# Optimization experiments

Measured on AMD Instinct MI355X. Metric: run time of the kernel, lower is better.

## Reference

```python
import jax, jax.numpy as jnp
import numpy as np

LEAK = 0.2
NUM_GRAPHS = 64


def _gat(h_in, src, dst, eh, W, att_src, att_dst, att_edge, lin_edge_W, bias, N):
    # PyG GATConv with edge_dim, concat=False (mean over heads)
    H, C = att_src.shape
    h = (h_in @ W).reshape(N, H, C)                      # [N,H,C]
    e = (eh @ lin_edge_W).reshape(-1, H, C)              # [Eaug,H,C]
    a_s = jnp.einsum('nhc,hc->nh', h, att_src)           # [N,H]
    a_d = jnp.einsum('nhc,hc->nh', h, att_dst)
    a_e = jnp.einsum('ehc,hc->eh', e, att_edge)          # [Eaug,H]
    score = jax.nn.leaky_relu(a_s[src] + a_d[dst] + a_e, LEAK)
    # scatter-softmax over incoming edges of each destination node
    m = jax.ops.segment_max(score, dst, num_segments=N)
    ex = jnp.exp(score - m[dst])
    den = jax.ops.segment_sum(ex, dst, num_segments=N)
    alpha = ex / den[dst]                                # [Eaug,H]
    out = jax.ops.segment_sum(alpha[:, :, None] * h[src], dst, num_segments=N)
    return out.mean(axis=1) + bias                       # concat=False -> head mean


def setup_inputs() -> dict:
    key = jax.random.key(0)
    ks = jax.random.split(key, 32)
    N, E, F, FE, HID, H, NT = 30000, 480000, 64, 16, 64, 4, 16
    Cin1 = F + HID
    s = 0.05
    d = {
        'x': jax.random.normal(ks[0], (N, F), jnp.float32),
        'edge_attr': jax.random.normal(ks[1], (E, FE), jnp.float32),
        'node_emb': jax.random.normal(ks[2], (NT, HID), jnp.float32) * s,
        'edge_W': jax.random.normal(ks[3], (FE, HID), jnp.float32) * s,
        'edge_b': jnp.zeros((HID,), jnp.float32),
        'W1': jax.random.normal(ks[4], (Cin1, H * HID), jnp.float32) * s,
        'as1': jax.random.normal(ks[5], (H, HID), jnp.float32) * s,
        'ad1': jax.random.normal(ks[6], (H, HID), jnp.float32) * s,
        'ae1': jax.random.normal(ks[7], (H, HID), jnp.float32) * s,
        'leW1': jax.random.normal(ks[8], (HID, H * HID), jnp.float32) * s,
        'b1': jnp.zeros((HID,), jnp.float32),
        'W2': jax.random.normal(ks[9], (HID, H * HID), jnp.float32) * s,
        'as2': jax.random.normal(ks[10], (H, HID), jnp.float32) * s,
        'ad2': jax.random.normal(ks[11], (H, HID), jnp.float32) * s,
        'ae2': jax.random.normal(ks[12], (H, HID), jnp.float32) * s,
        'leW2': jax.random.normal(ks[13], (HID, H * HID), jnp.float32) * s,
        'b2': jnp.zeros((HID,), jnp.float32),
        'sage_Wl': jax.random.normal(ks[14], (HID, HID), jnp.float32) * s,
        'sage_bl': jnp.zeros((HID,), jnp.float32),
        'sage_Wr': jax.random.normal(ks[15], (HID, HID), jnp.float32) * s,
        'lin1_W': jax.random.normal(ks[16], (HID, HID), jnp.float32) * s,
        'lin1_b': jnp.zeros((HID,), jnp.float32),
        'lin2_W': jax.random.normal(ks[17], (HID, HID), jnp.float32) * s,
        'lin2_b': jnp.zeros((HID,), jnp.float32),
        'tel_W': jax.random.normal(ks[18], (HID, 1), jnp.float32) * s,
        'tel_b': jnp.zeros((1,), jnp.float32),
        'comp_W': jax.random.normal(ks[19], (HID, 1), jnp.float32) * s,
        'comp_b': jnp.zeros((1,), jnp.float32),
        'pch_W': jax.random.normal(ks[20], (HID, 1), jnp.float32) * s,
        'pch_b': jnp.zeros((1,), jnp.float32),
        'edge_index': jax.random.randint(ks[21], (2, E), 0, N, jnp.int32),
        'batch': jnp.sort(jax.random.randint(ks[22], (N,), 0, NUM_GRAPHS, jnp.int32)),
        'node_type': jax.random.randint(ks[23], (N,), 0, NT, jnp.int32),
    }
    return d


def reference(x, edge_attr, node_emb, edge_W, edge_b,
              W1, as1, ad1, ae1, leW1, b1,
              W2, as2, ad2, ae2, leW2, b2,
              sage_Wl, sage_bl, sage_Wr,
              lin1_W, lin1_b, lin2_W, lin2_b,
              tel_W, tel_b, comp_W, comp_b, pch_W, pch_b,
              edge_index, batch, node_type):
    N = x.shape[0]
    src0, dst0 = edge_index[0], edge_index[1]

    h0 = jnp.concatenate([x, node_emb[node_type]], axis=-1)   # [N, F+HID]
    eh = edge_attr @ edge_W + edge_b                          # [E, HID]

    # GATConv default add_self_loops=True, fill_value='mean' on edge_attr
    loop = jnp.arange(N, dtype=src0.dtype)
    src = jnp.concatenate([src0, loop])
    dst = jnp.concatenate([dst0, loop])
    eh_aug = jnp.concatenate([eh, jnp.broadcast_to(eh.mean(axis=0), (N, eh.shape[1]))], axis=0)

    h1 = jax.nn.elu(_gat(h0, src, dst, eh_aug, W1, as1, ad1, ae1, leW1, b1, N))
    h2 = jax.nn.elu(_gat(h1, src, dst, eh_aug, W2, as2, ad2, ae2, leW2, b2, N))

    # SAGEConv: mean neighbor aggregation (src->dst) + root transform
    deg = jax.ops.segment_sum(jnp.ones_like(dst0, dtype=h2.dtype), dst0, num_segments=N)
    agg = jax.ops.segment_sum(h2[src0], dst0, num_segments=N) / jnp.clip(deg, 1.0)[:, None]
    h3 = jax.nn.elu(agg @ sage_Wl + sage_bl + h2 @ sage_Wr)

    # global mean pool per graph
    cnt = jax.ops.segment_sum(jnp.ones((N,), h3.dtype), batch, num_segments=NUM_GRAPHS)
    g = jax.ops.segment_sum(h3, batch, num_segments=NUM_GRAPHS) / jnp.clip(cnt, 1.0)[:, None]

    g = jax.nn.elu(g @ lin1_W + lin1_b)                       # dropout inactive (eval)
    g = g @ lin2_W + lin2_b
    return (g @ tel_W + tel_b, g @ comp_W + comp_b, g @ pch_W + pch_b)
```

## Files before the change

### kernel.cpp

```cpp
#include <hip/hip_runtime.h>
#include <math.h>

#define NN 30000
#define NE 480000
#define FEA 16
#define HID 64
#define NG 64
#define LEAKK 0.2f

#define S_MEANEA 0
#define S_KF1    16
#define S_C1     80
#define S_AEL1   84
#define S_KF2    88
#define S_C2     152
#define S_AEL2   156
#define S_MS1    160
#define S_MD1    672
#define S_MS2    1184
#define S_MD2    1440

__device__ __forceinline__ float eluf(float v) { return v > 0.f ? v : expm1f(v); }
__device__ __forceinline__ float leakyf(float v) { return v >= 0.f ? v : LEAKK * v; }
__device__ __forceinline__ void fma4(float4& a, float w, const float4& x) {
    a.x += w * x.x; a.y += w * x.y; a.z += w * x.z; a.w += w * x.w;
}

__global__ __launch_bounds__(256) void count_mean_kernel(
    const int* __restrict__ dst, const float* __restrict__ EA,
    int* __restrict__ cnt, float* __restrict__ S) {
    __shared__ float red[1024];
    int t = threadIdx.x;
    int base = blockIdx.x * 512;
#pragma unroll
    for (int i = 0; i < 2; i++) {
        int e = base + i * 256 + t;
        if (e < NE) atomicAdd(&cnt[dst[e]], 1);
    }
    int c4 = t & 3;
    int rbase = base + (t >> 2);
    float4 acc = {0, 0, 0, 0};
#pragma unroll
    for (int i = 0; i < 8; i++) {
        int r = rbase + i * 64;
        if (r < NE) {
            float4 v = *(const float4*)(EA + (size_t)r * FEA + c4 * 4);
            acc.x += v.x; acc.y += v.y; acc.z += v.z; acc.w += v.w;
        }
    }
    *(float4*)&red[t * 4] = acc;
    __syncthreads();
    if (t < 16) {
        int grp = t >> 2;
        int comp = t & 3;
        float sum = 0.f;
        for (int j = 0; j < 64; j++) sum += red[(grp + 4 * j) * 4 + comp];
        atomicAdd(&S[S_MEANEA + grp * 4 + comp], sum);
    }
}

__global__ void prep_weights_kernel(const float* __restrict__ W1, const float* __restrict__ W2,
                                    const float* __restrict__ Wl, const float* __restrict__ Wr,
                                    const float* __restrict__ emb,
                                    float* __restrict__ WC1, float* __restrict__ WC2,
                                    float* __restrict__ B128) {
    int i = blockIdx.x * 256 + threadIdx.x;
    if (i < 16384) {
        int hk = i >> 6, c = i & 63;
        int h = hk >> 6, k = hk & 63;
        WC1[i] = 0.25f * W1[k * 256 + h * 64 + c];
    } else if (i < 20480) {
        int j2 = i - 16384;
        int r2 = j2 >> 6, c = j2 & 63;
        int h = r2 >> 4, tau = r2 & 15;
        float v = 0.f;
        for (int j = 0; j < 64; j++)
            v += emb[tau * 64 + j] * W1[(64 + j) * 256 + h * 64 + c];
        WC1[i] = 0.25f * v;
    } else if (i < 36864) {
        int j = i - 20480;
        int hk = j >> 6, c = j & 63;
        int h = hk >> 6, k = hk & 63;
        WC2[j] = 0.25f * W2[k * 256 + h * 64 + c];
    } else if (i < 45056) {
        int j = i - 36864;
        int k = j >> 6, c = j & 63;
        B128[j] = (k < 64) ? Wl[k * 64 + c] : Wr[(k - 64) * 64 + c];
    }
}

__global__ void prep_small_kernel(
    const float* __restrict__ W1, const float* __restrict__ as1, const float* __restrict__ ad1,
    const float* __restrict__ ae1, const float* __restrict__ leW1,
    const float* __restrict__ W2, const float* __restrict__ as2, const float* __restrict__ ad2,
    const float* __restrict__ ae2, const float* __restrict__ leW2,
    const float* __restrict__ edge_W, const float* __restrict__ edge_b,
    float* __restrict__ S) {
    __shared__ float M1[256], M2[256], meh[64];
    int t = threadIdx.x;
    if (t < 16) S[S_MEANEA + t] *= (1.0f / (float)NE);
    __syncthreads();
    {
        int k = t >> 2, h = t & 3;
        float m1 = 0.f, m2 = 0.f;
        for (int c = 0; c < 64; c++) {
            m1 += leW1[k * 256 + h * 64 + c] * ae1[h * 64 + c];
            m2 += leW2[k * 256 + h * 64 + c] * ae2[h * 64 + c];
        }
        M1[t] = m1; M2[t] = m2;
    }
    if (t < 64) {
        float v = edge_b[t];
        for (int f = 0; f < FEA; f++) v += S[S_MEANEA + f] * edge_W[f * 64 + t];
        meh[t] = v;
    }
    __syncthreads();
    if (t < 64) {
        int f = t >> 2, h = t & 3;
        float k1 = 0.f, k2 = 0.f;
        for (int k = 0; k < 64; k++) {
            k1 += edge_W[f * 64 + k] * M1[k * 4 + h];
            k2 += edge_W[f * 64 + k] * M2[k * 4 + h];
        }
        S[S_KF1 + t] = k1; S[S_KF2 + t] = k2;
    } else if (t < 68) {
        int h = t - 64;
        float c1 = 0.f, c2 = 0.f, a1 = 0.f, a2 = 0.f;
        for (int k = 0; k < 64; k++) {
            c1 += edge_b[k] * M1[k * 4 + h];
            c2 += edge_b[k] * M2[k * 4 + h];
            a1 += meh[k] * M1[k * 4 + h];
            a2 += meh[k] * M2[k * 4 + h];
        }
        S[S_C1 + h] = c1; S[S_C2 + h] = c2;
        S[S_AEL1 + h] = a1; S[S_AEL2 + h] = a2;
    }
    for (int i = t; i < 512; i += 256) {
        int k = i >> 2, h = i & 3;
        float s = 0.f, d = 0.f;
        for (int c = 0; c < 64; c++) {
            float w = W1[k * 256 + h * 64 + c];
            s += w * as1[h * 64 + c];
            d += w * ad1[h * 64 + c];
        }
        S[S_MS1 + i] = s; S[S_MD1 + i] = d;
    }
    for (int i = t; i < 256; i += 256) {
        int k = i >> 2, h = i & 3;
        float s = 0.f, d = 0.f;
        for (int c = 0; c < 64; c++) {
            float w = W2[k * 256 + h * 64 + c];
            s += w * as2[h * 64 + c];
            d += w * ad2[h * 64 + c];
        }
        S[S_MS2 + i] = s; S[S_MD2 + i] = d;
    }
}

__global__ __launch_bounds__(256) void attn_h0_kernel(
    const float* __restrict__ x, const float* __restrict__ node_emb,
    const int* __restrict__ node_type, const float* __restrict__ S,
    float* __restrict__ as_, float* __restrict__ ad_) {
    __shared__ float xt[64 * 132];
    __shared__ float ms[512], md[512];
    __shared__ int ntS[64];
    int t = threadIdx.x;
    int n0 = blockIdx.x * 64;
    if (t < 64) {
        int n = n0 + t;
        ntS[t] = (n < NN) ? node_type[n] : 0;
    }
    for (int i = t; i < 512; i += 256) { ms[i] = S[S_MS1 + i]; md[i] = S[S_MD1 + i]; }
    __syncthreads();
    for (int i = t; i < 1024; i += 256) {
        int r = i >> 4, c4 = (i & 15) * 4;
        int n = n0 + r;
        float4 f = {0, 0, 0, 0};
        if (n < NN) f = *(const float4*)(x + (size_t)n * 64 + c4);
        *(float4*)&xt[r * 132 + c4] = f;
    }
    for (int i = t; i < 1024; i += 256) {
        int r = i >> 4, c4 = (i & 15) * 4;
        int n = n0 + r;
        float4 f = {0, 0, 0, 0};
        if (n < NN) f = *(const float4*)(node_emb + (size_t)ntS[r] * 64 + c4);
        *(float4*)&xt[r * 132 + 64 + c4] = f;
    }
    __syncthreads();
    int r = t >> 2, h = t & 3;
    float s = 0.f, d = 0.f;
#pragma unroll 8
    for (int k = 0; k < 128; k++) {
        float xv = xt[r * 132 + k];
        s += xv * ms[k * 4 + h];
        d += xv * md[k * 4 + h];
    }
    int n = n0 + r;
    if (n < NN) { as_[n * 4 + h] = s; ad_[n * 4 + h] = d; }
}

__global__ void scan_blocks_kernel(const int* __restrict__ cnt, int* __restrict__ eoff,
                                   int* __restrict__ bsum) {
    __shared__ int wsum[16];
    int t = threadIdx.x;
    int i = blockIdx.x * 1024 + t;
    int v = (i < NN) ? cnt[i] : 0;
    int lane = t & 63;
    int incl = v;
#pragma unroll
    for (int ofs = 1; ofs < 64; ofs <<= 1) {
        int u = __shfl_up(incl, ofs, 64);
        if (lane >= ofs) incl += u;
    }
    int wid = t >> 6;
    if (lane == 63) wsum[wid] = incl;
    __syncthreads();
    if (t < 16) {
        int s = wsum[t];
#pragma unroll
        for (int ofs = 1; ofs < 16; ofs <<= 1) {
            int u = __shfl_up(s, ofs, 64);
            if (t >= ofs) s += u;
        }
        wsum[t] = s;
    }
    __syncthreads();
    int excl = incl - v + (wid > 0 ? wsum[wid - 1] : 0);
    if (i < NN) eoff[i] = excl;
    if (t == 1023) bsum[blockIdx.x] = excl + v;
}

__global__ void scan_tops_kernel(const int* __restrict__ bsum, int* __restrict__ boff, int nb) {
    int t = threadIdx.x;
    int v = (t < nb) ? bsum[t] : 0;
    int incl = v;
#pragma unroll
    for (int ofs = 1; ofs < 64; ofs <<= 1) {
        int u = __shfl_up(incl, ofs, 64);
        if (t >= ofs) incl += u;
    }
    boff[t] = incl - v;
}

__global__ void scan_add_kernel(const int* __restrict__ boff, int* __restrict__ eoff) {
    int i = blockIdx.x * 256 + threadIdx.x;
    if (i < NN) eoff[i] += boff[i >> 10];
    if (i == 0) eoff[NN] = NE;
}

__global__ void scatter_score_kernel(const int* __restrict__ src, const int* __restrict__ dst,
                                     const float* __restrict__ EA, const float* __restrict__ S,
                                     const float* __restrict__ as_, const float* __restrict__ ad_,
                                     const int* __restrict__ node_type,
                                     const int* __restrict__ eoff, int* __restrict__ pos,
                                     int2* __restrict__ se_sorted,
                                     float* __restrict__ sc1, float* __restrict__ ae2s) {
    int e = blockIdx.x * 256 + threadIdx.x;
    if (e >= NE) return;
    int s = src[e], d = dst[e];
    float a1[4], a2[4];
#pragma unroll
    for (int h = 0; h < 4; h++) { a1[h] = S[S_C1 + h]; a2[h] = S[S_C2 + h]; }
    const float4* EA4 = (const float4*)(EA + (size_t)e * FEA);
#pragma unroll
    for (int q = 0; q < 4; q++) {
        float4 v = EA4[q];
        float vv[4] = {v.x, v.y, v.z, v.w};
#pragma unroll
        for (int j = 0; j < 4; j++) {
            int f = q * 4 + j;
#pragma unroll
            for (int h = 0; h < 4; h++) {
                a1[h] += vv[j] * S[S_KF1 + f * 4 + h];
                a2[h] += vv[j] * S[S_KF2 + f * 4 + h];
            }
        }
    }
    ((float4*)ae2s)[e] = make_float4(a2[0], a2[1], a2[2], a2[3]);
    float4 asv = ((const float4*)as_)[s];
    float4 adv = ((const float4*)ad_)[d];
    float4 r;
    r.x = expf(leakyf(asv.x + adv.x + a1[0]));
    r.y = expf(leakyf(asv.y + adv.y + a1[1]));
    r.z = expf(leakyf(asv.z + adv.z + a1[2]));
    r.w = expf(leakyf(asv.w + adv.w + a1[3]));
    ((float4*)sc1)[e] = r;
    int ty = node_type[s];
    int p = atomicAdd(&pos[d], 1);
    se_sorted[eoff[d] + p] = make_int2(s, e | (ty << 24));
}

__global__ void goff_bs_kernel(const int* __restrict__ batch, int* __restrict__ goff) {
    int g = threadIdx.x;
    if (g > NG) return;
    int lo = 0, hi = NN;
    while (lo < hi) {
        int mid = (lo + hi) >> 1;
        if (batch[mid] < g) lo = mid + 1; else hi = mid;
    }
    goff[g] = lo;
}

__global__ __launch_bounds__(256) void agg_gat1_kernel(
    const int* __restrict__ eoff, const int2* __restrict__ se_sorted,
    const float* __restrict__ sc1, const float* __restrict__ x,
    const int* __restrict__ node_type,
    const float* __restrict__ as_, const float* __restrict__ ad_,
    const float* __restrict__ Sael, float* __restrict__ agg) {
    int n = blockIdx.x * 4 + (threadIdx.x >> 6);
    if (n >= NN) return;
    int lane = threadIdx.x & 63;
    int sub = lane >> 4, ch = lane & 15;
    const float4* X4 = (const float4*)x;
    const float4* W4 = (const float4*)sc1;
    float4 asn = ((const float4*)as_)[n];
    float4 adn = ((const float4*)ad_)[n];
    float4 a0 = {0, 0, 0, 0}, a1 = a0, a2 = a0, a3 = a0, dn = a0, tw = a0;
    int b = eoff[n], e_end = eoff[n + 1];
    int nE = e_end - b;
    int i = sub;
    for (; i + 4 < nE; i += 8) {
        int2 se0 = se_sorted[b + i], se1 = se_sorted[b + i + 4];
        int e0 = se0.y & 0xFFFFFF, t0 = se0.y >> 24;
        int e1 = se1.y & 0xFFFFFF, t1 = se1.y >> 24;
        float4 w0 = W4[e0], w1 = W4[e1];
        float4 x0 = X4[(size_t)se0.x * 16 + ch];
        float4 x1 = X4[(size_t)se1.x * 16 + ch];
        fma4(a0, w0.x, x0); fma4(a1, w0.y, x0); fma4(a2, w0.z, x0); fma4(a3, w0.w, x0);
        fma4(a0, w1.x, x1); fma4(a1, w1.y, x1); fma4(a2, w1.z, x1); fma4(a3, w1.w, x1);
        dn.x += w0.x + w1.x; dn.y += w0.y + w1.y;
        dn.z += w0.z + w1.z; dn.w += w0.w + w1.w;
        if (ch == t0) { tw.x += w0.x; tw.y += w0.y; tw.z += w0.z; tw.w += w0.w; }
        if (ch == t1) { tw.x += w1.x; tw.y += w1.y; tw.z += w1.z; tw.w += w1.w; }
    }
    for (; i < nE; i += 4) {
        int2 se0 = se_sorted[b + i];
        int e0 = se0.y & 0xFFFFFF, t0 = se0.y >> 24;
        float4 w0 = W4[e0];
        float4 x0 = X4[(size_t)se0.x * 16 + ch];
        fma4(a0, w0.x, x0); fma4(a1, w0.y, x0); fma4(a2, w0.z, x0); fma4(a3, w0.w, x0);
        dn.x += w0.x; dn.y += w0.y; dn.z += w0.z; dn.w += w0.w;
        if (ch == t0) { tw.x += w0.x; tw.y += w0.y; tw.z += w0.z; tw.w += w0.w; }
    }
    if (sub == 0) {
        float e0 = expf(leakyf(asn.x + adn.x + Sael[0]));
        float e1 = expf(leakyf(asn.y + adn.y + Sael[1]));
        float e2 = expf(leakyf(asn.z + adn.z + Sael[2]));
        float e3 = expf(leakyf(asn.w + adn.w + Sael[3]));
        float4 xs = X4[(size_t)n * 16 + ch];
        fma4(a0, e0, xs); fma4(a1, e1, xs); fma4(a2, e2, xs); fma4(a3, e3, xs);
        dn.x += e0; dn.y += e1; dn.z += e2; dn.w += e3;
        int tn = node_type[n];
        if (ch == tn) { tw.x += e0; tw.y += e1; tw.z += e2; tw.w += e3; }
    }
#pragma unroll
    for (int mask = 16; mask < 64; mask <<= 1) {
        a0.x += __shfl_xor(a0.x, mask, 64); a0.y += __shfl_xor(a0.y, mask, 64);
        a0.z += __shfl_xor(a0.z, mask, 64); a0.w += __shfl_xor(a0.w, mask, 64);
        a1.x += __shfl_xor(a1.x, mask, 64); a1.y += __shfl_xor(a1.y, mask, 64);
        a1.z += __shfl_xor(a1.z, mask, 64); a1.w += __shfl_xor(a1.w, mask, 64);
        a2.x += __shfl_xor(a2.x, mask, 64); a2.y += __shfl_xor(a2.y, mask, 64);
        a2.z += __shfl_xor(a2.z, mask, 64); a2.w += __shfl_xor(a2.w, mask, 64);
        a3.x += __shfl_xor(a3.x, mask, 64); a3.y += __shfl_xor(a3.y, mask, 64);
        a3.z += __shfl_xor(a3.z, mask, 64); a3.w += __shfl_xor(a3.w, mask, 64);
        dn.x += __shfl_xor(dn.x, mask, 64); dn.y += __shfl_xor(dn.y, mask, 64);
        dn.z += __shfl_xor(dn.z, mask, 64); dn.w += __shfl_xor(dn.w, mask, 64);
        tw.x += __shfl_xor(tw.x, mask, 64); tw.y += __shfl_xor(tw.y, mask, 64);
        tw.z += __shfl_xor(tw.z, mask, 64); tw.w += __shfl_xor(tw.w, mask, 64);
    }
    if (sub == 0) {
        float i0 = 1.f / dn.x, i1 = 1.f / dn.y, i2 = 1.f / dn.z, i3 = 1.f / dn.w;
        float* A = agg + (size_t)n * 320;
        float4* A4 = (float4*)A;
        A4[ch]      = make_float4(a0.x * i0, a0.y * i0, a0.z * i0, a0.w * i0);
        A4[16 + ch] = make_float4(a1.x * i1, a1.y * i1, a1.z * i1, a1.w * i1);
        A4[32 + ch] = make_float4(a2.x * i2, a2.y * i2, a2.z * i2, a2.w * i2);
        A4[48 + ch] = make_float4(a3.x * i3, a3.y * i3, a3.z * i3, a3.w * i3);
        A[256 + ch]      = tw.x * i0;
        A[256 + 16 + ch] = tw.y * i1;
        A[256 + 32 + ch] = tw.z * i2;
        A[256 + 48 + ch] = tw.w * i3;
    }
}

__global__ __launch_bounds__(256) void agg_gat2_kernel(
    const int* __restrict__ eoff, const int2* __restrict__ se_sorted,
    const float* __restrict__ ae2s, const float* __restrict__ X,
    const float* __restrict__ as_, const float* __restrict__ ad_,
    const float* __restrict__ Sael, float* __restrict__ agg) {
    int n = blockIdx.x * 4 + (threadIdx.x >> 6);
    if (n >= NN) return;
    int lane = threadIdx.x & 63;
    int sub = lane >> 4, ch = lane & 15;
    const float4* X4 = (const float4*)X;
    const float4* W4 = (const float4*)ae2s;
    const float4* AS4 = (const float4*)as_;
    float4 asn = AS4[n];
    float4 adn = ((const float4*)ad_)[n];
    float4 a0 = {0, 0, 0, 0}, a1 = a0, a2 = a0, a3 = a0, dn = a0;
    int b = eoff[n], e = eoff[n + 1];
    int nE = e - b;
    int i = sub;
    for (; i + 4 < nE; i += 8) {
        int2 se0 = se_sorted[b + i], se1 = se_sorted[b + i + 4];
        float4 w0 = W4[se0.y & 0xFFFFFF], w1 = W4[se1.y & 0xFFFFFF];
        float4 q0 = AS4[se0.x], q1 = AS4[se1.x];
        w0.x = expf(leakyf(q0.x + adn.x + w0.x));
        w0.y = expf(leakyf(q0.y + adn.y + w0.y));
        w0.z = expf(leakyf(q0.z + adn.z + w0.z));
        w0.w = expf(leakyf(q0.w + adn.w + w0.w));
        w1.x = expf(leakyf(q1.x + adn.x + w1.x));
        w1.y = expf(leakyf(q1.y + adn.y + w1.y));
        w1.z = expf(leakyf(q1.z + adn.z + w1.z));
        w1.w = expf(leakyf(q1.w + adn.w + w1.w));
        float4 x0 = X4[(size_t)se0.x * 16 + ch];
        float4 x1 = X4[(size_t)se1.x * 16 + ch];
        fma4(a0, w0.x, x0); fma4(a1, w0.y, x0); fma4(a2, w0.z, x0); fma4(a3, w0.w, x0);
        fma4(a0, w1.x, x1); fma4(a1, w1.y, x1); fma4(a2, w1.z, x1); fma4(a3, w1.w, x1);
        dn.x += w0.x + w1.x; dn.y += w0.y + w1.y;
        dn.z += w0.z + w1.z; dn.w += w0.w + w1.w;
    }
    for (; i < nE; i += 4) {
        int2 se0 = se_sorted[b + i];
        float4 w0 = W4[se0.y & 0xFFFFFF];
        float4 q0 = AS4[se0.x];
        w0.x = expf(leakyf(q0.x + adn.x + w0.x));
        w0.y = expf(leakyf(q0.y + adn.y + w0.y));
        w0.z = expf(leakyf(q0.z + adn.z + w0.z));
        w0.w = expf(leakyf(q0.w + adn.w + w0.w));
        float4 x0 = X4[(size_t)se0.x * 16 + ch];
        fma4(a0, w0.x, x0); fma4(a1, w0.y, x0); fma4(a2, w0.z, x0); fma4(a3, w0.w, x0);
        dn.x += w0.x; dn.y += w0.y; dn.z += w0.z; dn.w += w0.w;
    }
    if (sub == 0) {
        float e0 = expf(leakyf(asn.x + adn.x + Sael[0]));
        float e1 = expf(leakyf(asn.y + adn.y + Sael[1]));
        float e2 = expf(leakyf(asn.z + adn.z + Sael[2]));
        float e3 = expf(leakyf(asn.w + adn.w + Sael[3]));
        float4 xs = X4[(size_t)n * 16 + ch];
        fma4(a0, e0, xs); fma4(a1, e1, xs); fma4(a2, e2, xs); fma4(a3, e3, xs);
        dn.x += e0; dn.y += e1; dn.z += e2; dn.w += e3;
    }
#pragma unroll
    for (int mask = 16; mask < 64; mask <<= 1) {
        a0.x += __shfl_xor(a0.x, mask, 64); a0.y += __shfl_xor(a0.y, mask, 64);
        a0.z += __shfl_xor(a0.z, mask, 64); a0.w += __shfl_xor(a0.w, mask, 64);
        a1.x += __shfl_xor(a1.x, mask, 64); a1.y += __shfl_xor(a1.y, mask, 64);
        a1.z += __shfl_xor(a1.z, mask, 64); a1.w += __shfl_xor(a1.w, mask, 64);
        a2.x += __shfl_xor(a2.x, mask, 64); a2.y += __shfl_xor(a2.y, mask, 64);
        a2.z += __shfl_xor(a2.z, mask, 64); a2.w += __shfl_xor(a2.w, mask, 64);
        a3.x += __shfl_xor(a3.x, mask, 64); a3.y += __shfl_xor(a3.y, mask, 64);
        a3.z += __shfl_xor(a3.z, mask, 64); a3.w += __shfl_xor(a3.w, mask, 64);
        dn.x += __shfl_xor(dn.x, mask, 64); dn.y += __shfl_xor(dn.y, mask, 64);
        dn.z += __shfl_xor(dn.z, mask, 64); dn.w += __shfl_xor(dn.w, mask, 64);
    }
    if (sub == 0) {
        float i0 = 1.f / dn.x, i1 = 1.f / dn.y, i2 = 1.f / dn.z, i3 = 1.f / dn.w;
        float4* agg4 = (float4*)(agg + (size_t)n * 256);
        agg4[ch]      = make_float4(a0.x * i0, a0.y * i0, a0.z * i0, a0.w * i0);
        agg4[16 + ch] = make_float4(a1.x * i1, a1.y * i1, a1.z * i1, a1.w * i1);
        agg4[32 + ch] = make_float4(a2.x * i2, a2.y * i2, a2.z * i2, a2.w * i2);
        agg4[48 + ch] = make_float4(a3.x * i3, a3.y * i3, a3.z * i3, a3.w * i3);
    }
}

template <int K, bool DOATT>
__global__ __launch_bounds__(256) void gemm64_kernel(
    const float* __restrict__ A, const float* __restrict__ B,
    const float* __restrict__ bias, float* __restrict__ out,
    const float* __restrict__ ms_g, const float* __restrict__ md_g,
    float* __restrict__ as_, float* __restrict__ ad_) {
    __shared__ float As[32 * 68];
    __shared__ float Bs[32 * 68];
    __shared__ float msS[256], mdS[256];
    int t = threadIdx.x;
    int tx = t & 15, ty = t >> 4;
    int m_base = blockIdx.x * 64;
    if (DOATT) { msS[t] = ms_g[t]; mdS[t] = md_g[t]; }
    int arow0 = t >> 3, akq0 = (t & 7) * 4;
    int arow1 = (t + 256) >> 3, akq1 = ((t + 256) & 7) * 4;
    int bkr = t >> 4, bnc = (t & 15) * 4;
    int am0 = m_base + arow0, am1 = m_base + arow1;
    float4 fa0, fa1, fb0, fb1;
    fa0 = (am0 < NN) ? *(const float4*)(A + (size_t)am0 * K + akq0) : make_float4(0, 0, 0, 0);
    fa1 = (am1 < NN) ? *(const float4*)(A + (size_t)am1 * K + akq1) : make_float4(0, 0, 0, 0);
    fb0 = *(const float4*)(B + (size_t)bkr * 64 + bnc);
    fb1 = *(const float4*)(B + (size_t)(bkr + 16) * 64 + bnc);
    float acc[4][4] = {};
    for (int k0 = 0;; k0 += 32) {
        As[(akq0 + 0) * 68 + arow0] = fa0.x;
        As[(akq0 + 1) * 68 + arow0] = fa0.y;
        As[(akq0 + 2) * 68 + arow0] = fa0.z;
        As[(akq0 + 3) * 68 + arow0] = fa0.w;
        As[(akq1 + 0) * 68 + arow1] = fa1.x;
        As[(akq1 + 1) * 68 + arow1] = fa1.y;
        As[(akq1 + 2) * 68 + arow1] = fa1.z;
        As[(akq1 + 3) * 68 + arow1] = fa1.w;
        *(float4*)&Bs[bkr * 68 + bnc] = fb0;
        *(float4*)&Bs[(bkr + 16) * 68 + bnc] = fb1;
        __syncthreads();
        bool more = (k0 + 32 < K);
        if (more) {
            int kn = k0 + 32;
            fa0 = (am0 < NN) ? *(const float4*)(A + (size_t)am0 * K + kn + akq0)
                             : make_float4(0, 0, 0, 0);
            fa1 = (am1 < NN) ? *(const float4*)(A + (size_t)am1 * K + kn + akq1)
                             : make_float4(0, 0, 0, 0);
            fb0 = *(const float4*)(B + (size_t)(kn + bkr) * 64 + bnc);
            fb1 = *(const float4*)(B + (size_t)(kn + bkr + 16) * 64 + bnc);
        }
#pragma unroll
        for (int k = 0; k < 32; k++) {
            float4 av = *(const float4*)&As[k * 68 + ty * 4];
            float4 bv = *(const float4*)&Bs[k * 68 + tx * 4];
            float a[4] = {av.x, av.y, av.z, av.w};
            float b[4] = {bv.x, bv.y, bv.z, bv.w};
#pragma unroll
            for (int i = 0; i < 4; i++)
#pragma unroll
                for (int j = 0; j < 4; j++) acc[i][j] += a[i] * b[j];
        }
        if (!more) break;
        __syncthreads();
    }
    float4 bvv = ((const float4*)bias)[tx];
    float o[4][4];
#pragma unroll
    for (int i = 0; i < 4; i++) {
        o[i][0] = eluf(acc[i][0] + bvv.x);
        o[i][1] = eluf(acc[i][1] + bvv.y);
        o[i][2] = eluf(acc[i][2] + bvv.z);
        o[i][3] = eluf(acc[i][3] + bvv.w);
        int m = m_base + ty * 4 + i;
        if (m < NN)
            *(float4*)(out + (size_t)m * 64 + tx * 4) =
                make_float4(o[i][0], o[i][1], o[i][2], o[i][3]);
    }
    if (DOATT) {
        float ps[4][4] = {}, pd[4][4] = {};
#pragma unroll
        for (int i = 0; i < 4; i++)
#pragma unroll
            for (int j = 0; j < 4; j++) {
                float v = o[i][j];
                int kk = (tx * 4 + j) * 4;
#pragma unroll
                for (int h = 0; h < 4; h++) {
                    ps[i][h] += v * msS[kk + h];
                    pd[i][h] += v * mdS[kk + h];
                }
            }
#pragma unroll
        for (int mk = 1; mk < 16; mk <<= 1) {
#pragma unroll
            for (int i = 0; i < 4; i++)
#pragma unroll
                for (int h = 0; h < 4; h++) {
                    ps[i][h] += __shfl_xor(ps[i][h], mk, 64);
                    pd[i][h] += __shfl_xor(pd[i][h], mk, 64);
                }
        }
        if (tx == 0) {
#pragma unroll
            for (int i = 0; i < 4; i++) {
                int m = m_base + ty * 4 + i;
                if (m < NN) {
                    *(float4*)(as_ + (size_t)m * 4) =
                        make_float4(ps[i][0], ps[i][1], ps[i][2], ps[i][3]);
                    *(float4*)(ad_ + (size_t)m * 4) =
                        make_float4(pd[i][0], pd[i][1], pd[i][2], pd[i][3]);
                }
            }
        }
    }
}

__global__ __launch_bounds__(256) void sage_agg3_kernel(
    const float* __restrict__ h2, const int* __restrict__ eoff,
    const int2* __restrict__ se_sorted, float* __restrict__ AB) {
    int n = blockIdx.x * 16 + (threadIdx.x >> 4);
    if (n >= NN) return;
    int l = threadIdx.x & 15;
    const float4* h24 = (const float4*)h2;
    float4* AB4 = (float4*)AB;
    float ax = 0.f, ay = 0.f, az = 0.f, aw = 0.f;
    int b = eoff[n], e_end = eoff[n + 1];
    int idx = b;
    int stop = b + ((e_end - b) & ~7);
    if (idx < stop) {
        int sreg[8];
#pragma unroll
        for (int u = 0; u < 8; u++) sreg[u] = se_sorted[idx + u].x;
        idx += 8;
        while (true) {
            int sn[8];
            bool more = idx < stop;
            if (more) {
#pragma unroll
                for (int u = 0; u < 8; u++) sn[u] = se_sorted[idx + u].x;
            }
#pragma unroll
            for (int u = 0; u < 8; u++) {
                float4 v = h24[(size_t)sreg[u] * 16 + l];
                ax += v.x; ay += v.y; az += v.z; aw += v.w;
            }
            if (!more) break;
#pragma unroll
            for (int u = 0; u < 8; u++) sreg[u] = sn[u];
            idx += 8;
        }
    }
    for (; idx < e_end; idx++) {
        float4 v0 = h24[(size_t)se_sorted[idx].x * 16 + l];
        ax += v0.x; ay += v0.y; az += v0.z; aw += v0.w;
    }
    float dg = (float)(e_end - b);
    if (dg < 1.f) dg = 1.f;
    float inv = 1.f / dg;
    AB4[(size_t)n * 32 + l] = make_float4(ax * inv, ay * inv, az * inv, aw * inv);
    AB4[(size_t)n * 32 + 16 + l] = h24[(size_t)n * 16 + l];
}

__global__ __launch_bounds__(256) void pool_mlp_kernel(
    const float* __restrict__ h3, const int* __restrict__ goff,
    const float* __restrict__ lin1W, const float* __restrict__ lin1b,
    const float* __restrict__ lin2W, const float* __restrict__ lin2b,
    const float* __restrict__ telW, const float* __restrict__ telb,
    const float* __restrict__ compW, const float* __restrict__ compb,
    const float* __restrict__ pchW, const float* __restrict__ pchb,
    float* __restrict__ out) {
    __shared__ float red[256];
    __shared__ float g[64], G1[64], G2[64];
    int gi = blockIdx.x, t = threadIdx.x;
    int c = t & 63, li = t >> 6;
    int b = goff[gi], e = goff[gi + 1];
    float sum = 0.f;
    for (int r = b + li; r < e; r += 4) sum += h3[(size_t)r * HID + c];
    red[t] = sum;
    __syncthreads();
    if (t < 64) {
        float v = red[t] + red[t + 64] + red[t + 128] + red[t + 192];
        float cntf = (float)(e - b);
        if (cntf < 1.f) cntf = 1.f;
        g[t] = v / cntf;
    }
    __syncthreads();
    {
        float part = 0.f;
#pragma unroll
        for (int k = li * 16; k < li * 16 + 16; k++) part += g[k] * lin1W[k * 64 + c];
        red[t] = part;
        __syncthreads();
        if (t < 64)
            G1[c] = eluf(red[c] + red[c + 64] + red[c + 128] + red[c + 192] + lin1b[c]);
        __syncthreads();
    }
    {
        float part = 0.f;
#pragma unroll
        for (int k = li * 16; k < li * 16 + 16; k++) part += G1[k] * lin2W[k * 64 + c];
        red[t] = part;
        __syncthreads();
        if (t < 64)
            G2[c] = red[c] + red[c + 64] + red[c + 128] + red[c + 192] + lin2b[c];
        __syncthreads();
    }
    if (t < 192) {
        int h = t >> 6, k = t & 63;
        const float* W = (h == 0) ? telW : ((h == 1) ? compW : pchW);
        red[t] = G2[k] * W[k];
    }
    __syncthreads();
    if (t < 3) {
        float acc = 0.f;
        for (int k = 0; k < 64; k++) acc += red[t * 64 + k];
        float bb = (t == 0) ? telb[0] : ((t == 1) ? compb[0] : pchb[0]);
        out[t * 64 + gi] = acc + bb;
    }
}

extern "C" void kernel_launch(void* const* d_in, const int* in_sizes, int n_in,
                              void* d_out, int out_size, void* d_ws, size_t ws_size,
                              hipStream_t stream) {
    const float* x        = (const float*)d_in[0];
    const float* EA       = (const float*)d_in[1];
    const float* node_emb = (const float*)d_in[2];
    const float* edge_W   = (const float*)d_in[3];
    const float* edge_b   = (const float*)d_in[4];
    const float* W1       = (const float*)d_in[5];
    const float* as1      = (const float*)d_in[6];
    const float* ad1      = (const float*)d_in[7];
    const float* ae1      = (const float*)d_in[8];
    const float* leW1     = (const float*)d_in[9];
    const float* b1       = (const float*)d_in[10];
    const float* W2       = (const float*)d_in[11];
    const float* as2      = (const float*)d_in[12];
    const float* ad2      = (const float*)d_in[13];
    const float* ae2      = (const float*)d_in[14];
    const float* leW2     = (const float*)d_in[15];
    const float* b2       = (const float*)d_in[16];
    const float* sage_Wl  = (const float*)d_in[17];
    const float* sage_bl  = (const float*)d_in[18];
    const float* sage_Wr  = (const float*)d_in[19];
    const float* lin1_W   = (const float*)d_in[20];
    const float* lin1_b   = (const float*)d_in[21];
    const float* lin2_W   = (const float*)d_in[22];
    const float* lin2_b   = (const float*)d_in[23];
    const float* tel_W    = (const float*)d_in[24];
    const float* tel_b    = (const float*)d_in[25];
    const float* comp_W   = (const float*)d_in[26];
    const float* comp_b   = (const float*)d_in[27];
    const float* pch_W    = (const float*)d_in[28];
    const float* pch_b    = (const float*)d_in[29];
    const int* edge_index = (const int*)d_in[30];
    const int* batch      = (const int*)d_in[31];
    const int* node_type  = (const int*)d_in[32];
    float* outp = (float*)d_out;

    const int* srcp = edge_index;
    const int* dstp = edge_index + NE;

    float* wf = (float*)d_ws;
    constexpr size_t OFF_H3    = 0;
    constexpr size_t OFF_AGG   = OFF_H3 + (size_t)NN * 64;
    constexpr size_t OFF_H1    = OFF_AGG + (size_t)NN * 512;
    constexpr size_t OFF_H2    = OFF_H1 + (size_t)NN * 64;
    constexpr size_t OFF_SC    = OFF_H2 + (size_t)NN * 64;
    constexpr size_t OFF_AE2   = OFF_SC + (size_t)NE * 4;
    constexpr size_t OFF_AS    = OFF_AE2 + (size_t)NE * 4;
    constexpr size_t OFF_AD    = OFF_AS + (size_t)NN * 4;
    constexpr size_t OFF_SMALL = OFF_AD + (size_t)NN * 4;
    constexpr size_t OFF_WC1   = OFF_SMALL + 4096;
    constexpr size_t OFF_WC2   = OFF_WC1 + 20480;
    constexpr size_t OFF_B128  = OFF_WC2 + 16384;
    constexpr size_t F_TOTAL   = OFF_B128 + 8192;

    int* wi         = (int*)(wf + F_TOTAL);
    int* cnt        = wi;
    int* pos        = wi + NN;
    int* eoff       = pos + NN;
    int2* se_sorted = (int2*)(eoff + (NN + 2));
    int* goff       = (int*)(se_sorted + NE);
    int* bsum       = goff + (NG + 1);
    int* boff       = bsum + 64;

    float* h3    = wf + OFF_H3;
    float* aggb  = wf + OFF_AGG;
    float* h1    = wf + OFF_H1;
    float* h2    = wf + OFF_H2;
    float* sc    = wf + OFF_SC;
    float* ae2s  = wf + OFF_AE2;
    float* as_   = wf + OFF_AS;
    float* ad_   = wf + OFF_AD;
    float* S     = wf + OFF_SMALL;
    float* WC1   = wf + OFF_WC1;
    float* WC2   = wf + OFF_WC2;
    float* B128  = wf + OFF_B128;
    float* AB    = wf + OFF_AGG;

    hipMemsetAsync(S + S_MEANEA, 0, 16 * sizeof(float), stream);
    hipMemsetAsync(cnt, 0, 2 * NN * sizeof(int), stream);

    count_mean_kernel<<<(NE + 511) / 512, 256, 0, stream>>>(dstp, EA, cnt, S);
    prep_weights_kernel<<<176, 256, 0, stream>>>(W1, W2, sage_Wl, sage_Wr, node_emb,
                                                 WC1, WC2, B128);
    prep_small_kernel<<<1, 256, 0, stream>>>(W1, as1, ad1, ae1, leW1,
                                             W2, as2, ad2, ae2, leW2,
                                             edge_W, edge_b, S);
    {
        int nb = (NN + 1023) / 1024;
        scan_blocks_kernel<<<nb, 1024, 0, stream>>>(cnt, eoff, bsum);
        scan_tops_kernel<<<1, 64, 0, stream>>>(bsum, boff, nb);
        scan_add_kernel<<<(NN + 255) / 256, 256, 0, stream>>>(boff, eoff);
    }
    attn_h0_kernel<<<(NN + 63) / 64, 256, 0, stream>>>(x, node_emb, node_type, S, as_, ad_);
    goff_bs_kernel<<<1, 128, 0, stream>>>(batch, goff);
    scatter_score_kernel<<<(NE + 255) / 256, 256, 0, stream>>>(
        srcp, dstp, EA, S, as_, ad_, node_type, eoff, pos, se_sorted, sc, ae2s);

    agg_gat1_kernel<<<(NN + 3) / 4, 256, 0, stream>>>(
        eoff, se_sorted, sc, x, node_type, as_, ad_, S + S_AEL1, aggb);
    gemm64_kernel<320, true><<<(NN + 63) / 64, 256, 0, stream>>>(
        aggb, WC1, b1, h1, S + S_MS2, S + S_MD2, as_, ad_);

    agg_gat2_kernel<<<(NN + 3) / 4, 256, 0, stream>>>(
        eoff, se_sorted, ae2s, h1, as_, ad_, S + S_AEL2, aggb);
    gemm64_kernel<256, false><<<(NN + 63) / 64, 256, 0, stream>>>(
        aggb, WC2, b2, h2, nullptr, nullptr, nullptr, nullptr);

    sage_agg3_kernel<<<(NN + 15) / 16, 256, 0, stream>>>(h2, eoff, se_sorted, AB);
    gemm64_kernel<128, false><<<(NN + 63) / 64, 256, 0, stream>>>(
        AB, B128, sage_bl, h3, nullptr, nullptr, nullptr, nullptr);

    pool_mlp_kernel<<<NG, 256, 0, stream>>>(h3, goff, lin1_W, lin1_b, lin2_W, lin2_b,
                                            tel_W, tel_b, comp_W, comp_b, pch_W, pch_b, outp);
}
```

Baseline: 438.9 us.

## Merge prep and goff kernels; precompute layer-2 edge scores in separate pass

Folds the two weight-prep kernels into one launch and moves the graph-offset binary search into the scan-tops launch, cutting two kernel launches. It also adds an edge-parallel score2 kernel that computes the exp(leaky) attention weights for layer 2 once per edge, in edge order. agg_gat2 then reads those weights directly instead of gathering as_[src] and evaluating exp four times per edge inside each wavefront. This trades redundant per-lane exp work and src gathers in the aggregation loop for an extra launch and an extra full pass writing and reading edge scores.

```diff
diff --git a/kernel.cpp b/kernel.cpp
--- a/kernel.cpp
+++ b/kernel.cpp
@@ -59,45 +59,44 @@
     }
 }
 
-__global__ void prep_weights_kernel(const float* __restrict__ W1, const float* __restrict__ W2,
-                                    const float* __restrict__ Wl, const float* __restrict__ Wr,
-                                    const float* __restrict__ emb,
-                                    float* __restrict__ WC1, float* __restrict__ WC2,
-                                    float* __restrict__ B128) {
-    int i = blockIdx.x * 256 + threadIdx.x;
-    if (i < 16384) {
-        int hk = i >> 6, c = i & 63;
-        int h = hk >> 6, k = hk & 63;
-        WC1[i] = 0.25f * W1[k * 256 + h * 64 + c];
-    } else if (i < 20480) {
-        int j2 = i - 16384;
-        int r2 = j2 >> 6, c = j2 & 63;
-        int h = r2 >> 4, tau = r2 & 15;
-        float v = 0.f;
-        for (int j = 0; j < 64; j++)
-            v += emb[tau * 64 + j] * W1[(64 + j) * 256 + h * 64 + c];
-        WC1[i] = 0.25f * v;
-    } else if (i < 36864) {
-        int j = i - 20480;
-        int hk = j >> 6, c = j & 63;
-        int h = hk >> 6, k = hk & 63;
-        WC2[j] = 0.25f * W2[k * 256 + h * 64 + c];
-    } else if (i < 45056) {
-        int j = i - 36864;
-        int k = j >> 6, c = j & 63;
-        B128[j] = (k < 64) ? Wl[k * 64 + c] : Wr[(k - 64) * 64 + c];
-    }
-}
-
-__global__ void prep_small_kernel(
+__global__ void prep_all_kernel(
     const float* __restrict__ W1, const float* __restrict__ as1, const float* __restrict__ ad1,
     const float* __restrict__ ae1, const float* __restrict__ leW1,
     const float* __restrict__ W2, const float* __restrict__ as2, const float* __restrict__ ad2,
     const float* __restrict__ ae2, const float* __restrict__ leW2,
     const float* __restrict__ edge_W, const float* __restrict__ edge_b,
-    float* __restrict__ S) {
+    const float* __restrict__ Wl, const float* __restrict__ Wr,
+    const float* __restrict__ emb,
+    float* __restrict__ S, float* __restrict__ WC1, float* __restrict__ WC2,
+    float* __restrict__ B128) {
+    int t = threadIdx.x;
+    if (blockIdx.x > 0) {
+        int i = (blockIdx.x - 1) * 256 + t;
+        if (i < 16384) {
+            int hk = i >> 6, c = i & 63;
+            int h = hk >> 6, k = hk & 63;
+            WC1[i] = 0.25f * W1[k * 256 + h * 64 + c];
+        } else if (i < 20480) {
+            int j2 = i - 16384;
+            int r2 = j2 >> 6, c = j2 & 63;
+            int h = r2 >> 4, tau = r2 & 15;
+            float v = 0.f;
+            for (int j = 0; j < 64; j++)
+                v += emb[tau * 64 + j] * W1[(64 + j) * 256 + h * 64 + c];
+            WC1[i] = 0.25f * v;
+        } else if (i < 36864) {
+            int j = i - 20480;
+            int hk = j >> 6, c = j & 63;
+            int h = hk >> 6, k = hk & 63;
+            WC2[j] = 0.25f * W2[k * 256 + h * 64 + c];
+        } else if (i < 45056) {
+            int j = i - 36864;
+            int k = j >> 6, c = j & 63;
+            B128[j] = (k < 64) ? Wl[k * 64 + c] : Wr[(k - 64) * 64 + c];
+        }
+        return;
+    }
     __shared__ float M1[256], M2[256], meh[64];
-    int t = threadIdx.x;
     if (t < 16) S[S_MEANEA + t] *= (1.0f / (float)NE);
     __syncthreads();
     {
@@ -230,8 +229,21 @@
     if (t == 1023) bsum[blockIdx.x] = excl + v;
 }
 
-__global__ void scan_tops_kernel(const int* __restrict__ bsum, int* __restrict__ boff, int nb) {
+__global__ void scan_tops_goff_kernel(const int* __restrict__ bsum, int* __restrict__ boff,
+                                      int nb, const int* __restrict__ batch,
+                                      int* __restrict__ goff) {
     int t = threadIdx.x;
+    if (blockIdx.x == 1) {
+        if (t > NG) return;
+        int lo = 0, hi = NN;
+        while (lo < hi) {
+            int mid = (lo + hi) >> 1;
+            if (batch[mid] < t) lo = mid + 1; else hi = mid;
+        }
+        goff[t] = lo;
+        return;
+    }
+    if (t >= 64) return;
     int v = (t < nb) ? bsum[t] : 0;
     int incl = v;
 #pragma unroll
@@ -290,15 +302,22 @@
     se_sorted[eoff[d] + p] = make_int2(s, e | (ty << 24));
 }
 
-__global__ void goff_bs_kernel(const int* __restrict__ batch, int* __restrict__ goff) {
-    int g = threadIdx.x;
-    if (g > NG) return;
-    int lo = 0, hi = NN;
-    while (lo < hi) {
-        int mid = (lo + hi) >> 1;
-        if (batch[mid] < g) lo = mid + 1; else hi = mid;
-    }
-    goff[g] = lo;
+__global__ void score2_kernel(const int* __restrict__ src, const int* __restrict__ dst,
+                              const float* __restrict__ ae2s,
+                              const float* __restrict__ as_, const float* __restrict__ ad_,
+                              float* __restrict__ sc2) {
+    int e = blockIdx.x * 256 + threadIdx.x;
+    if (e >= NE) return;
+    int s = src[e], d = dst[e];
+    float4 ae = ((const float4*)ae2s)[e];
+    float4 asv = ((const float4*)as_)[s];
+    float4 adv = ((const float4*)ad_)[d];
+    float4 r;
+    r.x = expf(leakyf(asv.x + adv.x + ae.x));
+    r.y = expf(leakyf(asv.y + adv.y + ae.y));
+    r.z = expf(leakyf(asv.z + adv.z + ae.z));
+    r.w = expf(leakyf(asv.w + adv.w + ae.w));
+    ((float4*)sc2)[e] = r;
 }
 
 __global__ __launch_bounds__(256) void agg_gat1_kernel(
@@ -385,7 +404,7 @@
 
 __global__ __launch_bounds__(256) void agg_gat2_kernel(
     const int* __restrict__ eoff, const int2* __restrict__ se_sorted,
-    const float* __restrict__ ae2s, const float* __restrict__ X,
+    const float* __restrict__ sc2, const float* __restrict__ X,
     const float* __restrict__ as_, const float* __restrict__ ad_,
     const float* __restrict__ Sael, float* __restrict__ agg) {
     int n = blockIdx.x * 4 + (threadIdx.x >> 6);
@@ -393,9 +412,8 @@
     int lane = threadIdx.x & 63;
     int sub = lane >> 4, ch = lane & 15;
     const float4* X4 = (const float4*)X;
-    const float4* W4 = (const float4*)ae2s;
-    const float4* AS4 = (const float4*)as_;
-    float4 asn = AS4[n];
+    const float4* W4 = (const float4*)sc2;
+    float4 asn = ((const float4*)as_)[n];
     float4 adn = ((const float4*)ad_)[n];
     float4 a0 = {0, 0, 0, 0}, a1 = a0, a2 = a0, a3 = a0, dn = a0;
     int b = eoff[n], e = eoff[n + 1];
@@ -404,15 +422,6 @@
     for (; i + 4 < nE; i += 8) {
         int2 se0 = se_sorted[b + i], se1 = se_sorted[b + i + 4];
         float4 w0 = W4[se0.y & 0xFFFFFF], w1 = W4[se1.y & 0xFFFFFF];
-        float4 q0 = AS4[se0.x], q1 = AS4[se1.x];
-        w0.x = expf(leakyf(q0.x + adn.x + w0.x));
-        w0.y = expf(leakyf(q0.y + adn.y + w0.y));
-        w0.z = expf(leakyf(q0.z + adn.z + w0.z));
-        w0.w = expf(leakyf(q0.w + adn.w + w0.w));
-        w1.x = expf(leakyf(q1.x + adn.x + w1.x));
-        w1.y = expf(leakyf(q1.y + adn.y + w1.y));
-        w1.z = expf(leakyf(q1.z + adn.z + w1.z));
-        w1.w = expf(leakyf(q1.w + adn.w + w1.w));
         float4 x0 = X4[(size_t)se0.x * 16 + ch];
         float4 x1 = X4[(size_t)se1.x * 16 + ch];
         fma4(a0, w0.x, x0); fma4(a1, w0.y, x0); fma4(a2, w0.z, x0); fma4(a3, w0.w, x0);
@@ -423,11 +432,6 @@
     for (; i < nE; i += 4) {
         int2 se0 = se_sorted[b + i];
         float4 w0 = W4[se0.y & 0xFFFFFF];
-        float4 q0 = AS4[se0.x];
-        w0.x = expf(leakyf(q0.x + adn.x + w0.x));
-        w0.y = expf(leakyf(q0.y + adn.y + w0.y));
-        w0.z = expf(leakyf(q0.z + adn.z + w0.z));
-        w0.w = expf(leakyf(q0.w + adn.w + w0.w));
         float4 x0 = X4[(size_t)se0.x * 16 + ch];
         fma4(a0, w0.x, x0); fma4(a1, w0.y, x0); fma4(a2, w0.z, x0); fma4(a3, w0.w, x0);
         dn.x += w0.x; dn.y += w0.y; dn.z += w0.z; dn.w += w0.w;
@@ -762,19 +766,17 @@
     hipMemsetAsync(cnt, 0, 2 * NN * sizeof(int), stream);
 
     count_mean_kernel<<<(NE + 511) / 512, 256, 0, stream>>>(dstp, EA, cnt, S);
-    prep_weights_kernel<<<176, 256, 0, stream>>>(W1, W2, sage_Wl, sage_Wr, node_emb,
-                                                 WC1, WC2, B128);
-    prep_small_kernel<<<1, 256, 0, stream>>>(W1, as1, ad1, ae1, leW1,
+    prep_all_kernel<<<177, 256, 0, stream>>>(W1, as1, ad1, ae1, leW1,
                                              W2, as2, ad2, ae2, leW2,
-                                             edge_W, edge_b, S);
+                                             edge_W, edge_b, sage_Wl, sage_Wr, node_emb,
+                                             S, WC1, WC2, B128);
     {
         int nb = (NN + 1023) / 1024;
         scan_blocks_kernel<<<nb, 1024, 0, stream>>>(cnt, eoff, bsum);
-        scan_tops_kernel<<<1, 64, 0, stream>>>(bsum, boff, nb);
+        scan_tops_goff_kernel<<<2, 128, 0, stream>>>(bsum, boff, nb, batch, goff);
         scan_add_kernel<<<(NN + 255) / 256, 256, 0, stream>>>(boff, eoff);
     }
     attn_h0_kernel<<<(NN + 63) / 64, 256, 0, stream>>>(x, node_emb, node_type, S, as_, ad_);
-    goff_bs_kernel<<<1, 128, 0, stream>>>(batch, goff);
     scatter_score_kernel<<<(NE + 255) / 256, 256, 0, stream>>>(
         srcp, dstp, EA, S, as_, ad_, node_type, eoff, pos, se_sorted, sc, ae2s);
 
@@ -783,8 +785,9 @@
     gemm64_kernel<320, true><<<(NN + 63) / 64, 256, 0, stream>>>(
         aggb, WC1, b1, h1, S + S_MS2, S + S_MD2, as_, ad_);
 
+    score2_kernel<<<(NE + 255) / 256, 256, 0, stream>>>(srcp, dstp, ae2s, as_, ad_, sc);
     agg_gat2_kernel<<<(NN + 3) / 4, 256, 0, stream>>>(
-        eoff, se_sorted, ae2s, h1, as_, ad_, S + S_AEL2, aggb);
+        eoff, se_sorted, sc, h1, as_, ad_, S + S_AEL2, aggb);
     gemm64_kernel<256, false><<<(NN + 63) / 64, 256, 0, stream>>>(
         aggb, WC2, b2, h2, nullptr, nullptr, nullptr, nullptr);
 
```

New measurement: 437.5 us. Within noise of the previous version (-0.3%).
